# Performance work log

Hardware: AMD Instinct MI355X
Metric: run time of the kernel (lower is better)

## Reference

```python
import jax, jax.numpy as jnp
import numpy as np


def setup_inputs() -> dict:
    key = jax.random.key(0)
    k1, k2 = jax.random.split(key)
    n_tokens, embed_dim, num_embed = 16384, 512, 2048
    encode = jax.random.normal(k1, (n_tokens, embed_dim), dtype=jnp.float32)
    # Embedding init in torch: uniform(-1/num_embed, 1/num_embed)
    templat = jax.random.uniform(
        k2, (num_embed, embed_dim), dtype=jnp.float32,
        minval=-1.0 / num_embed, maxval=1.0 / num_embed)
    return {"encode": encode, "templat": templat}


def reference(encode, templat):
    # match_encode_with_templat, eval path: sample=False, detach='encode', metric='l2'
    encode_d = jax.lax.stop_gradient(encode)
    # squared L2 distance: ||e||^2 - 2 e@t^T + ||t||^2 ; logits = -dist
    e_sq = jnp.sum(encode_d * encode_d, axis=-1, keepdims=True)       # (N, 1)
    t_sq = jnp.sum(templat * templat, axis=-1)[None, :]               # (1, M)
    dist = e_sq - 2.0 * (encode_d @ templat.T) + t_sq                 # (N, M)
    logits = -dist
    zsoft = jax.nn.softmax(logits, axis=-1)
    zidx = jnp.argmax(zsoft, axis=-1)                                 # (N,)
    quant = templat[zidx]                                             # (N, C) gather
    return quant, zidx
```

## Files before the change

kernel.cpp:

```cpp
#include <hip/hip_runtime.h>
#include <stdint.h>

#define N_TOK  16384
#define EMB    512
#define NEMB   2048
#define NCHUNK 32
#define CWIN   2.5e-4f
#define WCAP   524288

typedef __attribute__((ext_vector_type(8))) short s16x8;
typedef __attribute__((ext_vector_type(4))) float f32x4;

__device__ __forceinline__ unsigned short f2bf(float f) {
  unsigned u = __float_as_uint(f);
  u += 0x7fffu + ((u >> 16) & 1u);
  return (unsigned short)(u >> 16);
}
__device__ __forceinline__ unsigned mapf(float f) {
  unsigned u = __float_as_uint(f);
  return (u >> 31) ? ~u : (u | 0x80000000u);
}
__device__ __forceinline__ float unmapf(unsigned u) {
  return __uint_as_float((u >> 31) ? (u & 0x7fffffffu) : ~u);
}

template<int CTRL>
__device__ __forceinline__ float dppf(float x) {
  return __uint_as_float((unsigned)__builtin_amdgcn_update_dpp(
      0, (int)__float_as_uint(x), CTRL, 0xF, 0xF, true));
}
template<int CTRL>
__device__ __forceinline__ unsigned dppu(unsigned x) {
  return (unsigned)__builtin_amdgcn_update_dpp(0, (int)x, CTRL, 0xF, 0xF, true);
}

__device__ __forceinline__ float pairwise512_sq(const float* se, int lane) {
  int l = lane & 31;
  int b = l >> 3, j = l & 7;
  const float* base = se + b * 128 + j;
  float x = base[0];
  float r = __fmul_rn(x, x);
#pragma unroll
  for (int k = 1; k < 16; ++k) {
    float y = base[8 * k];
    r = __fadd_rn(r, __fmul_rn(y, y));
  }
  r = __fadd_rn(r, __shfl_xor(r, 1));
  r = __fadd_rn(r, __shfl_xor(r, 2));
  r = __fadd_rn(r, __shfl_xor(r, 4));
  r = __fadd_rn(r, __shfl_xor(r, 8));
  r = __fadd_rn(r, __shfl_xor(r, 16));
  return r;
}

__global__ __launch_bounds__(256) void prep_kernel(
    const float* __restrict__ tmp, const float* __restrict__ enc,
    unsigned short* __restrict__ thi, float* __restrict__ tsq,
    unsigned short* __restrict__ ehi, float* __restrict__ esq,
    int* __restrict__ wcount) {
  __shared__ float se[4][EMB];
  int wv = threadIdx.x >> 6, lane = threadIdx.x & 63;
  int row = blockIdx.x * 4 + wv;
  if (blockIdx.x == 0 && threadIdx.x == 0) *wcount = 0;
  bool isT = row < NEMB;
  const float* src = isT ? (tmp + (size_t)row * EMB)
                         : (enc + (size_t)(row - NEMB) * EMB);
  const float4* p = (const float4*)src + lane * 2;
  float4 v0 = p[0], v1 = p[1];
  float f[8] = {v0.x, v0.y, v0.z, v0.w, v1.x, v1.y, v1.z, v1.w};
  unsigned h[8];
#pragma unroll
  for (int i = 0; i < 8; ++i) { h[i] = f2bf(f[i]); se[wv][lane * 8 + i] = f[i]; }
  uint4 packed = { h[0] | (h[1] << 16), h[2] | (h[3] << 16),
                   h[4] | (h[5] << 16), h[6] | (h[7] << 16) };
  int lrow = isT ? row : row - NEMB;
  int blk = lrow >> 7, lr = lrow & 127;
  int kt = lane >> 2, cb = (lane & 3) * 16;
  char* base = (char*)(isT ? thi : ehi);
  *(uint4*)(base + (((size_t)(blk * 16 + kt)) << 13) + lr * 64 + cb) = packed;
  __syncthreads();
  float s = pairwise512_sq(se[wv], lane);
  if (lane == 0) { if (isT) tsq[row] = s; else esq[row - NEMB] = s; }
}

__global__ __launch_bounds__(256, 2) void score_kernel(
    const unsigned short* __restrict__ ehi, const unsigned short* __restrict__ thi,
    const float* __restrict__ tsq,
    unsigned long long* __restrict__ keyc, unsigned* __restrict__ s2c) {
  __shared__ __align__(16) char smem[73728];
  const int tid = threadIdx.x, w = tid >> 6, lane = tid & 63;
  const int q = lane >> 4, r = lane & 15;
  const int wr = w >> 1, wc = w & 1;
  const int tokb = (int)blockIdx.x >> 3;
  const int nbp  = (int)blockIdx.x & 7;

  const unsigned short* paA[2];
  const unsigned short* pbB[4];
#pragma unroll
  for (int i = 0; i < 2; ++i) {
    int Lp = i * 4096 + tid * 16;
    int P = Lp ^ (((Lp >> 7) & 3) << 4);
    paA[i] = (const unsigned short*)((const char*)ehi
             + (((size_t)tokb * 16) << 13) + (P >> 6) * 64 + (P & 63));
  }
#pragma unroll
  for (int i = 0; i < 4; ++i) {
    int Lp = i * 4096 + tid * 16;
    int P = Lp ^ (((Lp >> 7) & 3) << 4);
    int sub = P >> 13, rw = (P >> 6) & 127, cbyte = P & 63;
    pbB[i] = (const unsigned short*)((const char*)thi
             + (((size_t)((nbp * 2 + sub) * 16)) << 13) + rw * 64 + cbyte);
  }

#define GLD(src, dst)                                                    \
  __builtin_amdgcn_global_load_lds(                                      \
      (const __attribute__((address_space(1))) void*)(src),              \
      (__attribute__((address_space(3))) void*)(dst), 16, 0, 0)
#define STAGE(t) do {                                                    \
    char* da_ = smem + ((t) % 3) * 8192 + tid * 16;                      \
    char* db_ = smem + 24576 + ((t) % 3) * 16384 + tid * 16;             \
    GLD((const char*)paA[0] + (size_t)(t) * 8192, da_);                  \
    GLD((const char*)paA[1] + (size_t)(t) * 8192, da_ + 4096);           \
    GLD((const char*)pbB[0] + (size_t)(t) * 8192, db_);                  \
    GLD((const char*)pbB[1] + (size_t)(t) * 8192, db_ + 4096);           \
    GLD((const char*)pbB[2] + (size_t)(t) * 8192, db_ + 8192);           \
    GLD((const char*)pbB[3] + (size_t)(t) * 8192, db_ + 12288);          \
  } while (0)

  int offA[4], offB[8];
#pragma unroll
  for (int m = 0; m < 4; ++m) {
    int P = (wr * 64 + m * 16 + r) * 64 + q * 16;
    offA[m] = P ^ (((P >> 7) & 3) << 4);
  }
#pragma unroll
  for (int n = 0; n < 8; ++n) {
    int P = (wc * 128 + n * 16 + r) * 64 + q * 16;
    offB[n] = P ^ (((P >> 7) & 3) << 4);
  }

  f32x4 acc[4][8];
#pragma unroll
  for (int m = 0; m < 4; ++m)
#pragma unroll
    for (int n = 0; n < 8; ++n) acc[m][n] = (f32x4){0.f, 0.f, 0.f, 0.f};

  STAGE(0); STAGE(1);
  asm volatile("s_waitcnt vmcnt(6)" ::: "memory");
  __builtin_amdgcn_s_barrier();

#pragma unroll
  for (int t = 0; t < 16; ++t) {
    const char* Ab_ = smem + (t % 3) * 8192;
    const char* Bb_ = smem + 24576 + (t % 3) * 16384;
    if (t + 2 < 16) STAGE(t + 2);
    s16x8 af[4], bf[8];
#pragma unroll
    for (int m = 0; m < 4; ++m) af[m] = *(const s16x8*)(Ab_ + offA[m]);
#pragma unroll
    for (int n = 0; n < 8; ++n) bf[n] = *(const s16x8*)(Bb_ + offB[n]);
    __builtin_amdgcn_s_setprio(1);
#pragma unroll
    for (int n = 0; n < 8; ++n) {
      acc[0][n] = __builtin_amdgcn_mfma_f32_16x16x32_bf16(af[0], bf[n], acc[0][n], 0, 0, 0);
      acc[1][n] = __builtin_amdgcn_mfma_f32_16x16x32_bf16(af[1], bf[n], acc[1][n], 0, 0, 0);
      acc[2][n] = __builtin_amdgcn_mfma_f32_16x16x32_bf16(af[2], bf[n], acc[2][n], 0, 0, 0);
      acc[3][n] = __builtin_amdgcn_mfma_f32_16x16x32_bf16(af[3], bf[n], acc[3][n], 0, 0, 0);
    }
    __builtin_amdgcn_s_setprio(0);
    if (t < 14) { asm volatile("s_waitcnt vmcnt(6)" ::: "memory"); }
    else        { asm volatile("s_waitcnt vmcnt(0)" ::: "memory"); }
    __builtin_amdgcn_s_barrier();
  }

#define FOLD(CTRL) { float os_ = dppf<CTRL>(sb), os2_ = dppf<CTRL>(s2f);        \
    float mx_ = fmaxf(sb, os_);                                                 \
    s2f = fminf(fminf(s2f, os2_), mx_); sb = fminf(sb, os_); }
#define FOLDL(CTRL) { unsigned ol_ = dppu<CTRL>(li); li = li < ol_ ? li : ol_; }
#pragma unroll
  for (int nh = 0; nh < 2; ++nh) {
    const int chunk = nbp * 4 + wc * 2 + nh;
    const int nbase = chunk * 64;
    const float tq0 = tsq[nbase + r], tq1 = tsq[nbase + 16 + r],
                tq2 = tsq[nbase + 32 + r], tq3 = tsq[nbase + 48 + r];
#pragma unroll
    for (int m = 0; m < 4; ++m) {
      unsigned long long kk[4]; unsigned ss[4];
#pragma unroll
      for (int i = 0; i < 4; ++i) {
        float s0 = fmaf(-2.f, acc[m][nh * 4 + 0][i], tq0);
        float s1 = fmaf(-2.f, acc[m][nh * 4 + 1][i], tq1);
        float s2v = fmaf(-2.f, acc[m][nh * 4 + 2][i], tq2);
        float s3 = fmaf(-2.f, acc[m][nh * 4 + 3][i], tq3);
        float n01 = fminf(s0, s1), X01 = fmaxf(s0, s1);
        float n23 = fminf(s2v, s3), X23 = fmaxf(s2v, s3);
        float sb = fminf(n01, n23);
        float s2f = fminf(fminf(X01, X23), fmaxf(n01, n23));
        FOLD(0xB1) FOLD(0x4E) FOLD(0x124) FOLD(0x128)
        unsigned li = 0xFFFFFFFFu;
        li = (s3  == sb) ? (unsigned)(48 + r) : li;
        li = (s2v == sb) ? (unsigned)(32 + r) : li;
        li = (s1  == sb) ? (unsigned)(16 + r) : li;
        li = (s0  == sb) ? (unsigned)(r)      : li;
        FOLDL(0xB1) FOLDL(0x4E) FOLDL(0x124) FOLDL(0x128)
        kk[i] = ((unsigned long long)mapf(sb) << 32) | (unsigned)(nbase + (int)li);
        ss[i] = mapf(s2f);
      }
      if (r == 0) {
        size_t base = (size_t)chunk * N_TOK +
                      (size_t)(tokb * 128 + wr * 64 + m * 16 + q * 4);
        ((ulonglong2*)&keyc[base])[0] = make_ulonglong2(kk[0], kk[1]);
        ((ulonglong2*)&keyc[base])[1] = make_ulonglong2(kk[2], kk[3]);
        *(uint4*)&s2c[base] = make_uint4(ss[0], ss[1], ss[2], ss[3]);
      }
    }
  }
#undef FOLD
#undef FOLDL
#undef GLD
#undef STAGE
}

__global__ __launch_bounds__(256) void merge_kernel(
    const unsigned long long* __restrict__ keyc, const unsigned* __restrict__ s2c,
    int* __restrict__ bestIdx, int* __restrict__ flag, int* __restrict__ work,
    int* __restrict__ wcount, unsigned long long* __restrict__ rkey) {
  int t = blockIdx.x * 256 + threadIdx.x;
  if (t >= N_TOK) return;
  rkey[t] = ~0ULL;
  unsigned long long K = ~0ULL; unsigned S = 0xffffffffu;
  for (int c = 0; c < NCHUNK; ++c) {
    unsigned long long k = keyc[(size_t)c * N_TOK + t];
    unsigned s2 = s2c[(size_t)c * N_TOK + t];
    if (k < K) { unsigned o = (unsigned)(K >> 32); S = o < S ? o : S; K = k; }
    else { unsigned o = (unsigned)(k >> 32); S = o < S ? o : S; }
    S = s2 < S ? s2 : S;
  }
  float best_f   = unmapf((unsigned)(K >> 32));
  float second_f = unmapf(S);
  int idx = (int)(unsigned)(K & 0xffffffffu);
  bestIdx[t] = idx;
  bool ok = (second_f - best_f >= CWIN) && (idx >= 0) && (idx < NEMB) && (best_f == best_f);
  flag[t] = ok ? 0 : 1;
  if (!ok) {
    bool nanCase = !(best_f == best_f);
    float limit = best_f + CWIN;
    for (int c = 0; c < NCHUNK; ++c) {
      float cf = unmapf((unsigned)(keyc[(size_t)c * N_TOK + t] >> 32));
      if (nanCase || !(cf > limit)) {
        int pos = atomicAdd(wcount, 1);
        if (pos < WCAP) work[pos] = t * NCHUNK + c;
      }
    }
  }
}

__global__ __launch_bounds__(256) void refine_kernel(
    const float* __restrict__ enc, const float* __restrict__ tmp,
    const float* __restrict__ esq, const float* __restrict__ tsq,
    const int* __restrict__ work, const int* __restrict__ wcount,
    unsigned long long* __restrict__ rkey) {
  int total = *wcount; if (total > WCAP) total = WCAP;
  __shared__ float se[EMB];
  const int wv = threadIdx.x >> 6, lane = threadIdx.x & 63;
  const int g = lane >> 4, l16 = lane & 15;
  for (int p = blockIdx.x; p < total; p += gridDim.x) {
    __syncthreads();
    int item = work[p];
    int token = item / NCHUNK, c = item % NCHUNK;
    const float4* erow = (const float4*)(enc + (size_t)token * EMB);
    for (int i = threadIdx.x; i < 128; i += 256) ((float4*)se)[i] = erow[i];
    __syncthreads();
    float e2 = esq[token];
    unsigned long long lkey = ~0ULL;
#pragma unroll
    for (int j = 0; j < 4; ++j) {
      int m = c * 64 + wv * 16 + j * 4 + g;
      const float4* trow = (const float4*)(tmp + (size_t)m * EMB);
      double s = 0.0;
#pragma unroll
      for (int k = 0; k < 8; ++k) {
        float4 a = trow[l16 + 16 * k];
        float4 b = ((const float4*)se)[l16 + 16 * k];
        s += (double)a.x * b.x + (double)a.y * b.y
           + (double)a.z * b.z + (double)a.w * b.w;
      }
      s += __shfl_xor(s, 1); s += __shfl_xor(s, 2);
      s += __shfl_xor(s, 4); s += __shfl_xor(s, 8);
      if (l16 == 0) {
        float M  = (float)s;
        float d1 = __fadd_rn(e2, -__fmul_rn(2.0f, M));
        float d2 = __fadd_rn(d1, tsq[m]);
        unsigned long long key =
            ((unsigned long long)__float_as_uint(d2) << 32) | (unsigned)m;
        if (key < lkey) lkey = key;
      }
    }
    if (l16 == 0 && lkey != ~0ULL) atomicMin(&rkey[token], lkey);
  }
}

__global__ void gather_kernel(const float* __restrict__ tmp, const int* __restrict__ bestIdx,
                              const int* __restrict__ flag,
                              const unsigned long long* __restrict__ rkey,
                              float* __restrict__ out) {
  int token = blockIdx.x * 4 + (threadIdx.x >> 6);
  int lane = threadIdx.x & 63;
  int idx = flag[token] ? (int)(unsigned)(rkey[token] & 0xffffffffULL) : bestIdx[token];
  idx = idx < 0 ? 0 : (idx > NEMB - 1 ? NEMB - 1 : idx);
  const float4* src = (const float4*)(tmp + (size_t)idx * EMB) + lane * 2;
  float4* dst = (float4*)(out + (size_t)token * EMB) + lane * 2;
  dst[0] = src[0];
  dst[1] = src[1];
  if (lane == 0) out[(size_t)N_TOK * EMB + token] = (float)idx;
}

extern "C" void kernel_launch(void* const* d_in, const int* in_sizes, int n_in,
                              void* d_out, int out_size, void* d_ws, size_t ws_size,
                              hipStream_t stream) {
  const float* enc = (const float*)d_in[0];
  const float* tmp = (const float*)d_in[1];
  float* out = (float*)d_out;
  char* ws = (char*)d_ws;
  unsigned short* thi = (unsigned short*)ws;
  unsigned short* ehi = (unsigned short*)(ws + 2097152);
  float* tsq      = (float*)(ws + 18874368);
  float* esq      = (float*)(ws + 18882560);
  unsigned long long* keyc = (unsigned long long*)(ws + 18948096);
  unsigned* s2c   = (unsigned*)(ws + 23142400);
  int*   bestIdx  = (int*)  (ws + 25239552);
  int*   flag     = (int*)  (ws + 25305088);
  unsigned long long* rkey = (unsigned long long*)(ws + 25370624);
  int*   wcount   = (int*)  (ws + 25501696);
  int*   work     = (int*)  (ws + 25501760);

  prep_kernel  <<<4608,      256, 0, stream>>>(tmp, enc, thi, tsq, ehi, esq, wcount);
  score_kernel <<<1024,      256, 0, stream>>>(ehi, thi, tsq, keyc, s2c);
  merge_kernel <<<N_TOK/256, 256, 0, stream>>>(keyc, s2c, bestIdx, flag, work, wcount, rkey);
  refine_kernel<<<1024,      256, 0, stream>>>(enc, tmp, esq, tsq, work, wcount, rkey);
  gather_kernel<<<N_TOK/4,   256, 0, stream>>>(tmp, bestIdx, flag, rkey, out);
}
```

Measured before the change: 184.1 us.

## Fuse merge, refine and gather into one per-token finish kernel

Three kernels (merge, atomic work-queue refine, gather) are replaced by one finish kernel in which each wavefront owns a token. The wavefront reduces the 32 chunk keys with shuffles, recomputes ambiguous chunks in fp64 inline, and writes the gathered row. The chunk results are transposed to token-major layout so each token's 32 entries are contiguous. This removes two launches, the global atomic queue and the intermediate buffers, at the cost of scattered 8-byte stores in the score kernel and possible load imbalance when one token needs many refine chunks.

```diff
diff --git a/kernel.cpp b/kernel.cpp
--- a/kernel.cpp
+++ b/kernel.cpp
@@ -6,7 +6,6 @@
 #define NEMB   2048
 #define NCHUNK 32
 #define CWIN   2.5e-4f
-#define WCAP   524288
 
 typedef __attribute__((ext_vector_type(8))) short s16x8;
 typedef __attribute__((ext_vector_type(4))) float f32x4;
@@ -56,12 +55,10 @@
 __global__ __launch_bounds__(256) void prep_kernel(
     const float* __restrict__ tmp, const float* __restrict__ enc,
     unsigned short* __restrict__ thi, float* __restrict__ tsq,
-    unsigned short* __restrict__ ehi, float* __restrict__ esq,
-    int* __restrict__ wcount) {
+    unsigned short* __restrict__ ehi, float* __restrict__ esq) {
   __shared__ float se[4][EMB];
   int wv = threadIdx.x >> 6, lane = threadIdx.x & 63;
   int row = blockIdx.x * 4 + wv;
-  if (blockIdx.x == 0 && threadIdx.x == 0) *wcount = 0;
   bool isT = row < NEMB;
   const float* src = isT ? (tmp + (size_t)row * EMB)
                          : (enc + (size_t)(row - NEMB) * EMB);
@@ -207,11 +204,12 @@
         ss[i] = mapf(s2f);
       }
       if (r == 0) {
-        size_t base = (size_t)chunk * N_TOK +
-                      (size_t)(tokb * 128 + wr * 64 + m * 16 + q * 4);
-        ((ulonglong2*)&keyc[base])[0] = make_ulonglong2(kk[0], kk[1]);
-        ((ulonglong2*)&keyc[base])[1] = make_ulonglong2(kk[2], kk[3]);
-        *(uint4*)&s2c[base] = make_uint4(ss[0], ss[1], ss[2], ss[3]);
+        int token0 = tokb * 128 + wr * 64 + m * 16 + q * 4;
+#pragma unroll
+        for (int i = 0; i < 4; ++i) {
+          keyc[(size_t)(token0 + i) * NCHUNK + chunk] = kk[i];
+          s2c [(size_t)(token0 + i) * NCHUNK + chunk] = ss[i];
+        }
       }
     }
   }
@@ -221,98 +219,82 @@
 #undef STAGE
 }
 
-__global__ __launch_bounds__(256) void merge_kernel(
+__global__ __launch_bounds__(256) void finish_kernel(
+    const float* __restrict__ enc, const float* __restrict__ tmp,
+    const float* __restrict__ esq, const float* __restrict__ tsq,
     const unsigned long long* __restrict__ keyc, const unsigned* __restrict__ s2c,
-    int* __restrict__ bestIdx, int* __restrict__ flag, int* __restrict__ work,
-    int* __restrict__ wcount, unsigned long long* __restrict__ rkey) {
-  int t = blockIdx.x * 256 + threadIdx.x;
-  if (t >= N_TOK) return;
-  rkey[t] = ~0ULL;
-  unsigned long long K = ~0ULL; unsigned S = 0xffffffffu;
-  for (int c = 0; c < NCHUNK; ++c) {
-    unsigned long long k = keyc[(size_t)c * N_TOK + t];
-    unsigned s2 = s2c[(size_t)c * N_TOK + t];
-    if (k < K) { unsigned o = (unsigned)(K >> 32); S = o < S ? o : S; K = k; }
-    else { unsigned o = (unsigned)(k >> 32); S = o < S ? o : S; }
-    S = s2 < S ? s2 : S;
-  }
+    float* __restrict__ out) {
+  __shared__ float se[4][EMB];
+  const int wv = threadIdx.x >> 6, lane = threadIdx.x & 63;
+  const int g = lane >> 4, l16 = lane & 15;
+  const int t = blockIdx.x * 4 + wv;
+  unsigned long long myk = ~0ULL; unsigned mys = 0xffffffffu;
+  if (lane < 32) {
+    myk = keyc[(size_t)t * NCHUNK + lane];
+    mys = s2c[(size_t)t * NCHUNK + lane];
+  }
+  unsigned long long K = myk; unsigned S = mys;
+#pragma unroll
+  for (int mask = 1; mask < 32; mask <<= 1) {
+    unsigned long long ko = __shfl_xor(K, mask);
+    unsigned so = __shfl_xor(S, mask);
+    unsigned long long mx = K > ko ? K : ko;
+    unsigned hi = (unsigned)(mx >> 32);
+    K = K < ko ? K : ko;
+    S = S < so ? S : so;
+    S = hi < S ? hi : S;
+  }
+  K = __shfl(K, 0); S = __shfl(S, 0);
   float best_f   = unmapf((unsigned)(K >> 32));
   float second_f = unmapf(S);
   int idx = (int)(unsigned)(K & 0xffffffffu);
-  bestIdx[t] = idx;
   bool ok = (second_f - best_f >= CWIN) && (idx >= 0) && (idx < NEMB) && (best_f == best_f);
-  flag[t] = ok ? 0 : 1;
   if (!ok) {
+    const float4* erow = (const float4*)(enc + (size_t)t * EMB);
+    ((float4*)se[wv])[lane]      = erow[lane];
+    ((float4*)se[wv])[lane + 64] = erow[lane + 64];
+    float e2 = esq[t];
     bool nanCase = !(best_f == best_f);
     float limit = best_f + CWIN;
+    unsigned long long lkey = ~0ULL;
     for (int c = 0; c < NCHUNK; ++c) {
-      float cf = unmapf((unsigned)(keyc[(size_t)c * N_TOK + t] >> 32));
+      float cf = unmapf((unsigned)(__shfl(myk, c) >> 32));
       if (nanCase || !(cf > limit)) {
-        int pos = atomicAdd(wcount, 1);
-        if (pos < WCAP) work[pos] = t * NCHUNK + c;
+#pragma unroll
+        for (int j = 0; j < 16; ++j) {
+          int m = c * 64 + j * 4 + g;
+          const float4* trow = (const float4*)(tmp + (size_t)m * EMB);
+          double s = 0.0;
+#pragma unroll
+          for (int k = 0; k < 8; ++k) {
+            float4 a = trow[l16 + 16 * k];
+            float4 b = ((const float4*)se[wv])[l16 + 16 * k];
+            s += (double)a.x * b.x + (double)a.y * b.y
+               + (double)a.z * b.z + (double)a.w * b.w;
+          }
+          s += __shfl_xor(s, 1); s += __shfl_xor(s, 2);
+          s += __shfl_xor(s, 4); s += __shfl_xor(s, 8);
+          if (l16 == 0) {
+            float M  = (float)s;
+            float d1 = __fadd_rn(e2, -__fmul_rn(2.0f, M));
+            float d2 = __fadd_rn(d1, tsq[m]);
+            unsigned long long key =
+                ((unsigned long long)__float_as_uint(d2) << 32) | (unsigned)m;
+            if (key < lkey) lkey = key;
+          }
+        }
       }
     }
-  }
-}
-
-__global__ __launch_bounds__(256) void refine_kernel(
-    const float* __restrict__ enc, const float* __restrict__ tmp,
-    const float* __restrict__ esq, const float* __restrict__ tsq,
-    const int* __restrict__ work, const int* __restrict__ wcount,
-    unsigned long long* __restrict__ rkey) {
-  int total = *wcount; if (total > WCAP) total = WCAP;
-  __shared__ float se[EMB];
-  const int wv = threadIdx.x >> 6, lane = threadIdx.x & 63;
-  const int g = lane >> 4, l16 = lane & 15;
-  for (int p = blockIdx.x; p < total; p += gridDim.x) {
-    __syncthreads();
-    int item = work[p];
-    int token = item / NCHUNK, c = item % NCHUNK;
-    const float4* erow = (const float4*)(enc + (size_t)token * EMB);
-    for (int i = threadIdx.x; i < 128; i += 256) ((float4*)se)[i] = erow[i];
-    __syncthreads();
-    float e2 = esq[token];
-    unsigned long long lkey = ~0ULL;
-#pragma unroll
-    for (int j = 0; j < 4; ++j) {
-      int m = c * 64 + wv * 16 + j * 4 + g;
-      const float4* trow = (const float4*)(tmp + (size_t)m * EMB);
-      double s = 0.0;
-#pragma unroll
-      for (int k = 0; k < 8; ++k) {
-        float4 a = trow[l16 + 16 * k];
-        float4 b = ((const float4*)se)[l16 + 16 * k];
-        s += (double)a.x * b.x + (double)a.y * b.y
-           + (double)a.z * b.z + (double)a.w * b.w;
-      }
-      s += __shfl_xor(s, 1); s += __shfl_xor(s, 2);
-      s += __shfl_xor(s, 4); s += __shfl_xor(s, 8);
-      if (l16 == 0) {
-        float M  = (float)s;
-        float d1 = __fadd_rn(e2, -__fmul_rn(2.0f, M));
-        float d2 = __fadd_rn(d1, tsq[m]);
-        unsigned long long key =
-            ((unsigned long long)__float_as_uint(d2) << 32) | (unsigned)m;
-        if (key < lkey) lkey = key;
-      }
-    }
-    if (l16 == 0 && lkey != ~0ULL) atomicMin(&rkey[token], lkey);
-  }
-}
-
-__global__ void gather_kernel(const float* __restrict__ tmp, const int* __restrict__ bestIdx,
-                              const int* __restrict__ flag,
-                              const unsigned long long* __restrict__ rkey,
-                              float* __restrict__ out) {
-  int token = blockIdx.x * 4 + (threadIdx.x >> 6);
-  int lane = threadIdx.x & 63;
-  int idx = flag[token] ? (int)(unsigned)(rkey[token] & 0xffffffffULL) : bestIdx[token];
+    { unsigned long long o = __shfl_xor(lkey, 16); lkey = lkey < o ? lkey : o; }
+    { unsigned long long o = __shfl_xor(lkey, 32); lkey = lkey < o ? lkey : o; }
+    idx = (int)(unsigned)(lkey & 0xffffffffULL);
+  }
   idx = idx < 0 ? 0 : (idx > NEMB - 1 ? NEMB - 1 : idx);
   const float4* src = (const float4*)(tmp + (size_t)idx * EMB) + lane * 2;
-  float4* dst = (float4*)(out + (size_t)token * EMB) + lane * 2;
+  float4* dst = (float4*)(out + (size_t)t * EMB) + lane * 2;
   dst[0] = src[0];
   dst[1] = src[1];
-  if (lane == 0) out[(size_t)N_TOK * EMB + token] = (float)idx;
+  if (lane == 0) out[(size_t)N_TOK * EMB + t] = (float)idx;
 }
 
 extern "C" void kernel_launch(void* const* d_in, const int* in_sizes, int n_in,
@@ -328,15 +310,8 @@
   float* esq      = (float*)(ws + 18882560);
   unsigned long long* keyc = (unsigned long long*)(ws + 18948096);
   unsigned* s2c   = (unsigned*)(ws + 23142400);
-  int*   bestIdx  = (int*)  (ws + 25239552);
-  int*   flag     = (int*)  (ws + 25305088);
-  unsigned long long* rkey = (unsigned long long*)(ws + 25370624);
-  int*   wcount   = (int*)  (ws + 25501696);
-  int*   work     = (int*)  (ws + 25501760);
-
-  prep_kernel  <<<4608,      256, 0, stream>>>(tmp, enc, thi, tsq, ehi, esq, wcount);
-  score_kernel <<<1024,      256, 0, stream>>>(ehi, thi, tsq, keyc, s2c);
-  merge_kernel <<<N_TOK/256, 256, 0, stream>>>(keyc, s2c, bestIdx, flag, work, wcount, rkey);
-  refine_kernel<<<1024,      256, 0, stream>>>(enc, tmp, esq, tsq, work, wcount, rkey);
-  gather_kernel<<<N_TOK/4,   256, 0, stream>>>(tmp, bestIdx, flag, rkey, out);
-}
+
+  prep_kernel  <<<4608,     256, 0, stream>>>(tmp, enc, thi, tsq, ehi, esq);
+  score_kernel <<<1024,     256, 0, stream>>>(ehi, thi, tsq, keyc, s2c);
+  finish_kernel<<<N_TOK/4,  256, 0, stream>>>(enc, tmp, esq, tsq, keyc, s2c, out);
+}
```

Result: slower. 226.4 us (+22.9%).
